# Kernel optimization log

Hardware: AMD Instinct MI355X
Metric: run time of the kernel (lower is better)

The kernel has to match this reference:

```python
import jax, jax.numpy as jnp
import numpy as np

N, D_IN, D_H, D_OUT = 65536, 256, 256, 128
E, TOP_K = 16, 2


def setup_inputs() -> dict:
    key = jax.random.key(0)
    ks = jax.random.split(key, 16)
    s = 0.05
    inp = {
        'x': jax.random.normal(ks[0], (N, D_IN), jnp.float32),
        'W0': jax.random.normal(ks[1], (D_IN, D_H), jnp.float32) * s,
        'b0': jnp.zeros((D_H,), jnp.float32),
        'Wg1': jax.random.normal(ks[2], (D_H, E), jnp.float32) * s,
        'bg1': jnp.zeros((E,), jnp.float32),
        'We1': jax.random.normal(ks[3], (E, D_H, D_H), jnp.float32) * s,
        'be1': jnp.zeros((E, D_H), jnp.float32),
        'Wg2': jax.random.normal(ks[4], (D_H, E), jnp.float32) * s,
        'bg2': jnp.zeros((E,), jnp.float32),
        'We2': jax.random.normal(ks[5], (E, D_H, D_H), jnp.float32) * s,
        'be2': jnp.zeros((E, D_H), jnp.float32),
        'Wf': jax.random.normal(ks[6], (D_H, D_OUT), jnp.float32) * s,
        'bf': jnp.zeros((D_OUT,), jnp.float32),
    }
    return inp


def _moe_layer(h, Wg, bg, We, be):
    # naive gate: logits over experts, top-k, renormalized softmax of top-k vals
    logits = h @ Wg + bg                      # [N, E]
    gate_full = jax.nn.softmax(logits, axis=-1)  # returned 'gate' for std stat
    vals, idx = jax.lax.top_k(logits, TOP_K)  # [N, k]
    scores = jax.nn.softmax(vals, axis=-1)    # [N, k]
    # scatter top-k scores into dense combine weights [N, E]
    cw = (jax.nn.one_hot(idx, E, dtype=h.dtype) * scores[..., None]).sum(axis=1)
    # grouped GEMM expressed as masked per-expert GEMMs (E is small, fixed)
    y = jnp.zeros((h.shape[0], We.shape[-1]), h.dtype)
    for e in range(E):
        y = y + cw[:, e:e + 1] * (h @ We[e] + be[e])
    # torch.std defaults to unbiased (ddof=1)
    gate_std_mean = jnp.std(gate_full, axis=1, ddof=1).mean()
    return y, gate_std_mean


def reference(x, W0, b0, Wg1, bg1, We1, be1, Wg2, bg2, We2, be2, Wf, bf):
    h = jax.nn.relu(x @ W0 + b0)
    h, g1 = _moe_layer(h, Wg1, bg1, We1, be1)
    h = jax.nn.relu(h)
    h, g2 = _moe_layer(h, Wg2, bg2, We2, be2)
    h = jax.nn.relu(h)
    out = h @ Wf + bf
    gate_std_means_mean = (g1 + g2) * 0.5
    return out, gate_std_means_mean
```

## Files before the change

kernel.cpp:

```cpp
#include <hip/hip_runtime.h>
#include <math.h>

#define NT 65536
#define DH 256
#define DO 128
#define NE 16
#define MAXCH 528
#define CPX 66

struct RInfo { int e1, e2; float s1, s2; };

typedef __attribute__((ext_vector_type(8))) short bh8;
typedef __attribute__((ext_vector_type(4))) float fx4;

static __device__ __forceinline__ short f2bf(float f) {
    union { float f; unsigned u; } v; v.f = f;
    return (short)((v.u + 0x7FFFu + ((v.u >> 16) & 1u)) >> 16);
}

template<bool RELU>
__global__ __launch_bounds__(256)
void gemm_dense(const float* __restrict__ A, const float* __restrict__ B,
                const float* __restrict__ bias, float* __restrict__ C,
                int ncols)
{
    __shared__ float As[128][36];
    __shared__ float Bs[32][132];
    const int tid = threadIdx.x;
    const int tx = tid & 15, ty = tid >> 4;
    const int rowBase = blockIdx.x * 128;
    const int colBase = blockIdx.y * 128;

    float acc[8][8];
#pragma unroll
    for (int i = 0; i < 8; ++i)
#pragma unroll
        for (int j = 0; j < 8; ++j) acc[i][j] = 0.f;

    for (int kt = 0; kt < DH; kt += 32) {
        {
            const int r = tid >> 3, k4 = (tid & 7) << 2;
#pragma unroll
            for (int it = 0; it < 4; ++it) {
                const float4 v = *reinterpret_cast<const float4*>(
                    &A[(size_t)(rowBase + r + 32 * it) * DH + kt + k4]);
                *reinterpret_cast<float4*>(&As[r + 32 * it][k4]) = v;
            }
        }
        {
            const int kr = tid >> 5, c4 = (tid & 31) << 2;
#pragma unroll
            for (int it = 0; it < 4; ++it) {
                const float4 v = *reinterpret_cast<const float4*>(
                    &B[(size_t)(kt + kr + 8 * it) * ncols + colBase + c4]);
                *reinterpret_cast<float4*>(&Bs[kr + 8 * it][c4]) = v;
            }
        }
        __syncthreads();
#pragma unroll
        for (int k4 = 0; k4 < 32; k4 += 4) {
            alignas(16) float ar[8][4];
#pragma unroll
            for (int i = 0; i < 8; ++i)
                *reinterpret_cast<float4*>(ar[i]) =
                    *reinterpret_cast<const float4*>(&As[ty * 8 + i][k4]);
#pragma unroll
            for (int kk = 0; kk < 4; ++kk) {
                alignas(16) float br[8];
                *reinterpret_cast<float4*>(&br[0]) =
                    *reinterpret_cast<const float4*>(&Bs[k4 + kk][tx * 8]);
                *reinterpret_cast<float4*>(&br[4]) =
                    *reinterpret_cast<const float4*>(&Bs[k4 + kk][tx * 8 + 4]);
#pragma unroll
                for (int i = 0; i < 8; ++i) {
                    const float a = ar[i][kk];
#pragma unroll
                    for (int j = 0; j < 8; ++j)
                        acc[i][j] = fmaf(a, br[j], acc[i][j]);
                }
            }
        }
        __syncthreads();
    }
    alignas(16) float bb[8];
#pragma unroll
    for (int j = 0; j < 8; ++j) bb[j] = bias[colBase + tx * 8 + j];
#pragma unroll
    for (int i = 0; i < 8; ++i) {
        const size_t row = rowBase + ty * 8 + i;
        alignas(16) float o[8];
#pragma unroll
        for (int j = 0; j < 8; ++j) {
            float v = acc[i][j] + bb[j];
            if (RELU) v = fmaxf(v, 0.f);
            o[j] = v;
        }
        float* p = &C[row * (size_t)ncols + colBase + tx * 8];
        *reinterpret_cast<float4*>(p)     = *reinterpret_cast<float4*>(&o[0]);
        *reinterpret_cast<float4*>(p + 4) = *reinterpret_cast<float4*>(&o[4]);
    }
}

__global__ __launch_bounds__(256)
void gate_kernel(const float* __restrict__ H, const float* __restrict__ Wg,
                 const float* __restrict__ bg, RInfo* __restrict__ info,
                 float* gsum, int* __restrict__ bc0, int* __restrict__ bc1)
{
    __shared__ float wgsT[16][260];
    __shared__ float hs[16][260];
    __shared__ float lg[16][17];
    __shared__ float sbg[16];
    __shared__ float sds[16];
    __shared__ int hh0[NE], hh1[NE];
    const int tid = threadIdx.x;
    const int rowBase = blockIdx.x * 16;

#pragma unroll
    for (int it = 0; it < 4; ++it) {
        const int flat = (tid + 256 * it) * 4;
        const int k = flat >> 4, e4 = flat & 15;
        const float4 v = *reinterpret_cast<const float4*>(&Wg[flat]);
        wgsT[e4 + 0][k] = v.x;
        wgsT[e4 + 1][k] = v.y;
        wgsT[e4 + 2][k] = v.z;
        wgsT[e4 + 3][k] = v.w;
    }
    if (tid < 16) { sbg[tid] = bg[tid]; hh0[tid] = 0; hh1[tid] = 0; }
#pragma unroll
    for (int it = 0; it < 4; ++it) {
        const int flat = (tid + 256 * it) * 4;
        const int r = flat >> 8, k = flat & 255;
        *reinterpret_cast<float4*>(&hs[r][k]) =
            *reinterpret_cast<const float4*>(&H[(size_t)(rowBase + r) * DH + k]);
    }
    __syncthreads();
    {
        const int r = tid >> 4, e = tid & 15;
        float acc = 0.f;
#pragma unroll 8
        for (int k = 0; k < 256; k += 4) {
            const float4 hv = *reinterpret_cast<const float4*>(&hs[r][k]);
            const float4 wv = *reinterpret_cast<const float4*>(&wgsT[e][k]);
            acc = fmaf(hv.x, wv.x, acc);
            acc = fmaf(hv.y, wv.y, acc);
            acc = fmaf(hv.z, wv.z, acc);
            acc = fmaf(hv.w, wv.w, acc);
        }
        lg[r][e] = acc + sbg[e];
    }
    __syncthreads();
    if (tid < 16) {
        const int row = rowBase + tid;
        float l[16];
#pragma unroll
        for (int i = 0; i < 16; ++i) l[i] = lg[tid][i];
        int i1 = 0; float v1 = l[0];
#pragma unroll
        for (int i = 1; i < 16; ++i) if (l[i] > v1) { v1 = l[i]; i1 = i; }
        int i2 = -1; float v2 = -INFINITY;
#pragma unroll
        for (int i = 0; i < 16; ++i) if (i != i1 && l[i] > v2) { v2 = l[i]; i2 = i; }
        const float t = expf(v2 - v1);
        const float s1 = 1.f / (1.f + t);
        const float s2 = t / (1.f + t);
        float p[16]; float S = 0.f;
#pragma unroll
        for (int i = 0; i < 16; ++i) { p[i] = expf(l[i] - v1); S += p[i]; }
        const float inv = 1.f / S;
        float sq = 0.f;
#pragma unroll
        for (int i = 0; i < 16; ++i) { const float q = p[i] * inv; sq = fmaf(q, q, sq); }
        const float var = (sq - 1.0f / 16.0f) * (1.0f / 15.0f);
        const float sd = sqrtf(fmaxf(var, 0.f));

        RInfo ri; ri.e1 = i1; ri.e2 = i2; ri.s1 = s1; ri.s2 = s2;
        info[row] = ri;
        sds[tid] = sd;
        atomicAdd(&hh0[i1], 1);
        atomicAdd(&hh1[i2], 1);
    }
    __syncthreads();
    if (tid == 0) {
        float s = 0.f;
#pragma unroll
        for (int i = 0; i < 16; ++i) s += sds[i];
        atomicAdd(gsum, s);
    }
    if (tid < 16) {
        const int b = blockIdx.x >> 4;
        if (hh0[tid]) atomicAdd(&bc0[tid * 256 + b], hh0[tid]);
        if (hh1[tid]) atomicAdd(&bc1[tid * 256 + b], hh1[tid]);
    }
}

__global__ void zero_meta(int* bc0, int* bc1, float* gsum)
{
    const int idx = blockIdx.x * 256 + threadIdx.x;
    bc0[idx] = 0; bc1[idx] = 0;
    if (idx < 2) gsum[idx] = 0.f;
}

__global__ void scan2_kernel(int* __restrict__ bc0, int* __restrict__ bc1,
                             int* cnt0, int* cnt1, int* off0, int* off1,
                             int* __restrict__ bo0, int* __restrict__ bo1)
{
    __shared__ int tot0[NE], tot1[NE], base0[NE], base1[NE];
    const int t = threadIdx.x;
    if (t < NE) {
        int s = 0;
        for (int b = 0; b < 256; ++b) s += bc0[t * 256 + b];
        tot0[t] = s; cnt0[t] = s;
    } else if (t < 2 * NE) {
        const int e = t - NE;
        int s = 0;
        for (int b = 0; b < 256; ++b) s += bc1[e * 256 + b];
        tot1[e] = s; cnt1[e] = s;
    }
    __syncthreads();
    if (t == 0) { int a = 0; for (int e = 0; e < NE; ++e) { base0[e] = a; off0[e] = a; a += tot0[e]; } }
    if (t == 1) { int a = 0; for (int e = 0; e < NE; ++e) { base1[e] = a; off1[e] = a; a += tot1[e]; } }
    __syncthreads();
    if (t < NE) {
        int run = base0[t];
        for (int b = 0; b < 256; ++b) { bo0[t * 256 + b] = run; run += bc0[t * 256 + b]; }
    } else if (t < 2 * NE) {
        const int e = t - NE;
        int run = base1[e];
        for (int b = 0; b < 256; ++b) { bo1[e * 256 + b] = run; run += bc1[e * 256 + b]; }
    }
    __syncthreads();
    for (int i = t; i < NE * 256; i += 64) { bc0[i] = 0; bc1[i] = 0; }
}

__global__ __launch_bounds__(256)
void scatter2_kernel(const RInfo* __restrict__ info, const int* __restrict__ bo0,
                     const int* __restrict__ bo1, int* __restrict__ l0,
                     int* __restrict__ l1)
{
    __shared__ int h0[NE], h1[NE];
    const int tid = threadIdx.x, b = blockIdx.x;
    if (tid < NE) { h0[tid] = 0; h1[tid] = 0; }
    __syncthreads();
    const int r = b * 256 + tid;
    const RInfo ri = info[r];
    const int p0 = atomicAdd(&h0[ri.e1], 1);
    const int p1 = atomicAdd(&h1[ri.e2], 1);
    l0[bo0[ri.e1 * 256 + b] + p0] = r;
    l1[bo1[ri.e2 * 256 + b] + p1] = r;
}

template<int SLOT>
__global__ __launch_bounds__(256)
void gemm_expert(const float* __restrict__ Hin, const float* __restrict__ We,
                 const float* __restrict__ be, const RInfo* __restrict__ info,
                 const int* __restrict__ list, const int* __restrict__ cnts,
                 const int* __restrict__ offs, float* __restrict__ P,
                 short* __restrict__ Ybf)
{
    __shared__ float As[128][36];
    __shared__ float Bs[32][132];
    __shared__ int   rs[128];
    __shared__ float ss[128];

    int c = (blockIdx.x & 7) * CPX + (blockIdx.x >> 3);
    int e;
    int cnt = 0;
    for (e = 0; e < NE; ++e) {
        cnt = cnts[e];
        const int nch = (cnt + 127) >> 7;
        if (c < nch) break;
        c -= nch;
    }
    if (e >= NE) return;
    const int m = min(128, cnt - c * 128);
    const int base = offs[e] + c * 128;
    const int tid = threadIdx.x;
    const int tx = tid & 15, ty = tid >> 4;
    const int colBase = blockIdx.y * 128;

    if (tid < 128) {
        const int g = list[base + min(tid, m - 1)];
        rs[tid] = g;
        const RInfo ri = info[g];
        ss[tid] = (SLOT == 0) ? ri.s1 : ri.s2;
    }
    __syncthreads();

    const float* B = We + (size_t)e * DH * DH;

    float acc[8][8];
#pragma unroll
    for (int i = 0; i < 8; ++i)
#pragma unroll
        for (int j = 0; j < 8; ++j) acc[i][j] = 0.f;

    for (int kt = 0; kt < DH; kt += 32) {
        {
            const int r = tid >> 3, k4 = (tid & 7) << 2;
#pragma unroll
            for (int it = 0; it < 4; ++it) {
                const int g = rs[r + 32 * it];
                const float4 v = *reinterpret_cast<const float4*>(
                    &Hin[(size_t)g * DH + kt + k4]);
                *reinterpret_cast<float4*>(&As[r + 32 * it][k4]) = v;
            }
        }
        {
            const int kr = tid >> 5, c4 = (tid & 31) << 2;
#pragma unroll
            for (int it = 0; it < 4; ++it) {
                const float4 v = *reinterpret_cast<const float4*>(
                    &B[(size_t)(kt + kr + 8 * it) * DH + colBase + c4]);
                *reinterpret_cast<float4*>(&Bs[kr + 8 * it][c4]) = v;
            }
        }
        __syncthreads();
#pragma unroll
        for (int k4 = 0; k4 < 32; k4 += 4) {
            alignas(16) float ar[8][4];
#pragma unroll
            for (int i = 0; i < 8; ++i)
                *reinterpret_cast<float4*>(ar[i]) =
                    *reinterpret_cast<const float4*>(&As[ty * 8 + i][k4]);
#pragma unroll
            for (int kk = 0; kk < 4; ++kk) {
                alignas(16) float br[8];
                *reinterpret_cast<float4*>(&br[0]) =
                    *reinterpret_cast<const float4*>(&Bs[k4 + kk][tx * 8]);
                *reinterpret_cast<float4*>(&br[4]) =
                    *reinterpret_cast<const float4*>(&Bs[k4 + kk][tx * 8 + 4]);
#pragma unroll
                for (int i = 0; i < 8; ++i) {
                    const float a = ar[i][kk];
#pragma unroll
                    for (int j = 0; j < 8; ++j)
                        acc[i][j] = fmaf(a, br[j], acc[i][j]);
                }
            }
        }
        __syncthreads();
    }

    alignas(16) float bb[8];
#pragma unroll
    for (int j = 0; j < 8; ++j) bb[j] = be[(size_t)e * DH + colBase + tx * 8 + j];
#pragma unroll
    for (int i = 0; i < 8; ++i) {
        const int rl = ty * 8 + i;
        if (rl < m) {
            const int g = rs[rl];
            const float s = ss[rl];
            alignas(16) float o[8];
#pragma unroll
            for (int j = 0; j < 8; ++j) o[j] = s * (acc[i][j] + bb[j]);
            float* pp = &P[(size_t)g * DH + colBase + tx * 8];
            if (SLOT == 0) {
                *reinterpret_cast<float4*>(pp)     = *reinterpret_cast<float4*>(&o[0]);
                *reinterpret_cast<float4*>(pp + 4) = *reinterpret_cast<float4*>(&o[4]);
            } else {
                const float4 p0 = *reinterpret_cast<const float4*>(pp);
                const float4 p1 = *reinterpret_cast<const float4*>(pp + 4);
                alignas(16) float h[8];
                h[0] = fmaxf(o[0] + p0.x, 0.f); h[1] = fmaxf(o[1] + p0.y, 0.f);
                h[2] = fmaxf(o[2] + p0.z, 0.f); h[3] = fmaxf(o[3] + p0.w, 0.f);
                h[4] = fmaxf(o[4] + p1.x, 0.f); h[5] = fmaxf(o[5] + p1.y, 0.f);
                h[6] = fmaxf(o[6] + p1.z, 0.f); h[7] = fmaxf(o[7] + p1.w, 0.f);
                *reinterpret_cast<float4*>(pp)     = *reinterpret_cast<float4*>(&h[0]);
                *reinterpret_cast<float4*>(pp + 4) = *reinterpret_cast<float4*>(&h[4]);
                if (Ybf) {
                    bh8 yb;
#pragma unroll
                    for (int j = 0; j < 8; ++j) yb[j] = f2bf(h[j]);
                    *reinterpret_cast<bh8*>(&Ybf[(size_t)g * DH + colBase + tx * 8]) = yb;
                }
            }
        }
    }
}

__global__ __launch_bounds__(256)
void transp_bf16(const float* __restrict__ W, short* __restrict__ WT,
                 int K, int N)
{
    __shared__ float t[32][33];
    const int k0 = blockIdx.x * 32, n0 = blockIdx.y * 32;
    const size_t off = (size_t)blockIdx.z * K * N;
    const int c = threadIdx.x & 31, r8 = threadIdx.x >> 5;
#pragma unroll
    for (int it = 0; it < 4; ++it) {
        const int r = r8 + it * 8;
        t[r][c] = W[off + (size_t)(k0 + r) * N + n0 + c];
    }
    __syncthreads();
#pragma unroll
    for (int it = 0; it < 4; ++it) {
        const int r = r8 + it * 8;
        WT[off + (size_t)(n0 + r) * K + k0 + c] = f2bf(t[c][r]);
    }
}

template<int SLOT, int BFA>
__global__ __launch_bounds__(256)
void gemm_expert_bf16(const float* __restrict__ Yf, const short* __restrict__ Abf,
                      const short* __restrict__ WeT,
                      const float* __restrict__ be, const RInfo* __restrict__ info,
                      const int* __restrict__ list, const int* __restrict__ cnts,
                      const int* __restrict__ offs, float* __restrict__ P,
                      short* __restrict__ Hbf)
{
    __shared__ bh8 As8[512];
    __shared__ bh8 Bs8[512];
    __shared__ int   rs[128];
    __shared__ float ss[128];

    int c = (blockIdx.x & 7) * CPX + (blockIdx.x >> 3);
    int e;
    int cnt = 0;
    for (e = 0; e < NE; ++e) {
        cnt = cnts[e];
        const int nch = (cnt + 127) >> 7;
        if (c < nch) break;
        c -= nch;
    }
    if (e >= NE) return;
    const int m = min(128, cnt - c * 128);
    const int base = offs[e] + c * 128;
    const int tid = threadIdx.x;

    if (tid < 128) {
        const int g = list[base + min(tid, m - 1)];
        rs[tid] = g;
        const RInfo ri = info[g];
        ss[tid] = (SLOT == 0) ? ri.s1 : ri.s2;
    }
    __syncthreads();

    const int colBase = blockIdx.y * 128;
    const int lane = tid & 63, wave = tid >> 6;
    const int wr = wave >> 1, wc = wave & 1;
    const short* Bw = WeT + (size_t)e * DH * DH;

    fx4 acc[4][4];
    const fx4 z = {0.f, 0.f, 0.f, 0.f};
#pragma unroll
    for (int i = 0; i < 4; ++i)
#pragma unroll
        for (int j = 0; j < 4; ++j) acc[i][j] = z;

    const int d0 = tid, d1 = tid + 256;
    const int ar0 = d0 >> 2, ak0 = d0 & 3;
    const int ar1 = d1 >> 2, ak1 = d1 & 3;
    const int g0 = ar0 * 4 + (ak0 ^ ((ar0 >> 1) & 3));
    const int g1 = ar1 * 4 + (ak1 ^ ((ar1 >> 1) & 3));
    const size_t arow0 = (size_t)rs[ar0] * DH, arow1 = (size_t)rs[ar1] * DH;
    const size_t brow0 = (size_t)(colBase + ar0) * DH, brow1 = (size_t)(colBase + ar1) * DH;

    for (int kt = 0; kt < DH; kt += 32) {
        if (BFA) {
            As8[g0] = *reinterpret_cast<const bh8*>(&Abf[arow0 + kt + ak0 * 8]);
            As8[g1] = *reinterpret_cast<const bh8*>(&Abf[arow1 + kt + ak1 * 8]);
        } else {
            const float* s0 = &Yf[arow0 + kt + ak0 * 8];
            const float4 f0 = *reinterpret_cast<const float4*>(s0);
            const float4 f1 = *reinterpret_cast<const float4*>(s0 + 4);
            bh8 v;
            v[0]=f2bf(f0.x); v[1]=f2bf(f0.y); v[2]=f2bf(f0.z); v[3]=f2bf(f0.w);
            v[4]=f2bf(f1.x); v[5]=f2bf(f1.y); v[6]=f2bf(f1.z); v[7]=f2bf(f1.w);
            As8[g0] = v;
            const float* s1 = &Yf[arow1 + kt + ak1 * 8];
            const float4 f2 = *reinterpret_cast<const float4*>(s1);
            const float4 f3 = *reinterpret_cast<const float4*>(s1 + 4);
            bh8 w;
            w[0]=f2bf(f2.x); w[1]=f2bf(f2.y); w[2]=f2bf(f2.z); w[3]=f2bf(f2.w);
            w[4]=f2bf(f3.x); w[5]=f2bf(f3.y); w[6]=f2bf(f3.z); w[7]=f2bf(f3.w);
            As8[g1] = w;
        }
        {
            Bs8[g0] = *reinterpret_cast<const bh8*>(&Bw[brow0 + kt + ak0 * 8]);
            Bs8[g1] = *reinterpret_cast<const bh8*>(&Bw[brow1 + kt + ak1 * 8]);
        }
        __syncthreads();
        const int kq = lane >> 4, lm = lane & 15;
        bh8 af[4], bfr[4];
#pragma unroll
        for (int i = 0; i < 4; ++i) {
            const int rl = wr * 64 + i * 16 + lm;
            af[i] = As8[rl * 4 + (kq ^ ((rl >> 1) & 3))];
            const int cl = wc * 64 + i * 16 + lm;
            bfr[i] = Bs8[cl * 4 + (kq ^ ((cl >> 1) & 3))];
        }
#pragma unroll
        for (int i = 0; i < 4; ++i)
#pragma unroll
            for (int j = 0; j < 4; ++j)
                acc[i][j] = __builtin_amdgcn_mfma_f32_16x16x32_bf16(
                    af[i], bfr[j], acc[i][j], 0, 0, 0);
        __syncthreads();
    }

    const int rq = lane >> 4, lm = lane & 15;
#pragma unroll
    for (int i = 0; i < 4; ++i) {
#pragma unroll
        for (int j = 0; j < 4; ++j) {
            const int rl = wr * 64 + i * 16 + rq * 4 + j;
            if (rl < m) {
                const int g = rs[rl];
                const float s = ss[rl];
#pragma unroll
                for (int nf = 0; nf < 4; ++nf) {
                    const int cl = colBase + wc * 64 + nf * 16 + lm;
                    float* pp = &P[(size_t)g * DH + cl];
                    const float o = s * (acc[i][nf][j] + be[(size_t)e * DH + cl]);
                    if (SLOT == 0) {
                        *pp = o;
                    } else {
                        const float v = fmaxf(*pp + o, 0.f);
                        if (BFA) Hbf[(size_t)g * DH + cl] = f2bf(v);
                        else     *pp = v;
                    }
                }
            }
        }
    }
}

template<int BFA>
__global__ __launch_bounds__(256)
void gemm_final_bf16(const float* __restrict__ Hf, const short* __restrict__ Habf,
                     const short* __restrict__ WT,
                     const float* __restrict__ bias, float* __restrict__ C,
                     const float* gsum, float* scalar_out)
{
    __shared__ bh8 As8[512];
    __shared__ bh8 Bs8[512];
    const int tid = threadIdx.x;
    const int rowBase = blockIdx.x * 128;

    if (blockIdx.x == 0 && tid == 0)
        *scalar_out = (gsum[0] + gsum[1]) * (0.5f / (float)NT);

    const int lane = tid & 63, wave = tid >> 6;
    const int wr = wave >> 1, wc = wave & 1;

    fx4 acc[4][4];
    const fx4 z = {0.f, 0.f, 0.f, 0.f};
#pragma unroll
    for (int i = 0; i < 4; ++i)
#pragma unroll
        for (int j = 0; j < 4; ++j) acc[i][j] = z;

    const int d0 = tid, d1 = tid + 256;
    const int ar0 = d0 >> 2, ak0 = d0 & 3;
    const int ar1 = d1 >> 2, ak1 = d1 & 3;
    const int g0 = ar0 * 4 + (ak0 ^ ((ar0 >> 1) & 3));
    const int g1 = ar1 * 4 + (ak1 ^ ((ar1 >> 1) & 3));
    const size_t arow0 = (size_t)(rowBase + ar0) * DH, arow1 = (size_t)(rowBase + ar1) * DH;
    const size_t brow0 = (size_t)ar0 * DH, brow1 = (size_t)ar1 * DH;

    for (int kt = 0; kt < DH; kt += 32) {
        if (BFA) {
            As8[g0] = *reinterpret_cast<const bh8*>(&Habf[arow0 + kt + ak0 * 8]);
            As8[g1] = *reinterpret_cast<const bh8*>(&Habf[arow1 + kt + ak1 * 8]);
        } else {
            const float* s0 = &Hf[arow0 + kt + ak0 * 8];
            const float4 f0 = *reinterpret_cast<const float4*>(s0);
            const float4 f1 = *reinterpret_cast<const float4*>(s0 + 4);
            bh8 v;
            v[0]=f2bf(f0.x); v[1]=f2bf(f0.y); v[2]=f2bf(f0.z); v[3]=f2bf(f0.w);
            v[4]=f2bf(f1.x); v[5]=f2bf(f1.y); v[6]=f2bf(f1.z); v[7]=f2bf(f1.w);
            As8[g0] = v;
            const float* s1 = &Hf[arow1 + kt + ak1 * 8];
            const float4 f2 = *reinterpret_cast<const float4*>(s1);
            const float4 f3 = *reinterpret_cast<const float4*>(s1 + 4);
            bh8 w;
            w[0]=f2bf(f2.x); w[1]=f2bf(f2.y); w[2]=f2bf(f2.z); w[3]=f2bf(f2.w);
            w[4]=f2bf(f3.x); w[5]=f2bf(f3.y); w[6]=f2bf(f3.z); w[7]=f2bf(f3.w);
            As8[g1] = w;
        }
        {
            Bs8[g0] = *reinterpret_cast<const bh8*>(&WT[brow0 + kt + ak0 * 8]);
            Bs8[g1] = *reinterpret_cast<const bh8*>(&WT[brow1 + kt + ak1 * 8]);
        }
        __syncthreads();
        const int kq = lane >> 4, lm = lane & 15;
        bh8 af[4], bfr[4];
#pragma unroll
        for (int i = 0; i < 4; ++i) {
            const int rl = wr * 64 + i * 16 + lm;
            af[i] = As8[rl * 4 + (kq ^ ((rl >> 1) & 3))];
            const int cl = wc * 64 + i * 16 + lm;
            bfr[i] = Bs8[cl * 4 + (kq ^ ((cl >> 1) & 3))];
        }
#pragma unroll
        for (int i = 0; i < 4; ++i)
#pragma unroll
            for (int j = 0; j < 4; ++j)
                acc[i][j] = __builtin_amdgcn_mfma_f32_16x16x32_bf16(
                    af[i], bfr[j], acc[i][j], 0, 0, 0);
        __syncthreads();
    }

    const int rq = lane >> 4, lm = lane & 15;
#pragma unroll
    for (int i = 0; i < 4; ++i) {
#pragma unroll
        for (int j = 0; j < 4; ++j) {
            const int rl = rowBase + wr * 64 + i * 16 + rq * 4 + j;
#pragma unroll
            for (int nf = 0; nf < 4; ++nf) {
                const int cl = wc * 64 + nf * 16 + lm;
                C[(size_t)rl * DO + cl] = acc[i][nf][j] + bias[cl];
            }
        }
    }
}

extern "C" void kernel_launch(void* const* d_in, const int* in_sizes, int n_in,
                              void* d_out, int out_size, void* d_ws, size_t ws_size,
                              hipStream_t stream)
{
    const float* x   = (const float*)d_in[0];
    const float* W0  = (const float*)d_in[1];
    const float* b0  = (const float*)d_in[2];
    const float* Wg1 = (const float*)d_in[3];
    const float* bg1 = (const float*)d_in[4];
    const float* We1 = (const float*)d_in[5];
    const float* be1 = (const float*)d_in[6];
    const float* Wg2 = (const float*)d_in[7];
    const float* bg2 = (const float*)d_in[8];
    const float* We2 = (const float*)d_in[9];
    const float* be2 = (const float*)d_in[10];
    const float* Wf  = (const float*)d_in[11];
    const float* bf  = (const float*)d_in[12];
    float* out = (float*)d_out;

    char* w = (char*)d_ws;
    float* H    = (float*)w; w += (size_t)NT * DH * 4;
    float* Y    = (float*)w; w += (size_t)NT * DH * 4;
    RInfo* info = (RInfo*)w; w += (size_t)NT * sizeof(RInfo);
    int* l0   = (int*)w; w += (size_t)NT * 4;
    int* l1   = (int*)w; w += (size_t)NT * 4;
    int* bc0  = (int*)w; w += NE * 256 * 4;
    int* bc1  = (int*)w; w += NE * 256 * 4;
    int* bo0  = (int*)w; w += NE * 256 * 4;
    int* bo1  = (int*)w; w += NE * 256 * 4;
    int* cnt0 = (int*)w; w += 64;
    int* cnt1 = (int*)w; w += 64;
    int* off0 = (int*)w; w += 64;
    int* off1 = (int*)w; w += 64;
    float* gsum = (float*)w; w += 64;
    short* WeT = (short*)w; w += (size_t)NE * DH * DH * 2;
    short* WfT = (short*)w; w += (size_t)DH * DO * 2;
    short* Ybf = (short*)w; w += (size_t)NT * DH * 2;
    const bool roomy = (size_t)(w - (char*)d_ws) <= ws_size;
    short* Hbf = (short*)Y;

    zero_meta<<<dim3(16), dim3(256), 0, stream>>>(bc0, bc1, gsum);
    transp_bf16<<<dim3(8, 8, 16), dim3(256), 0, stream>>>(We2, WeT, DH, DH);
    transp_bf16<<<dim3(8, 4, 1),  dim3(256), 0, stream>>>(Wf,  WfT, DH, DO);

    gemm_dense<true><<<dim3(NT / 128, 2), dim3(256), 0, stream>>>(x, W0, b0, H, DH);

    gate_kernel<<<dim3(NT / 16), dim3(256), 0, stream>>>(H, Wg1, bg1, info, &gsum[0], bc0, bc1);
    scan2_kernel<<<dim3(1), dim3(64), 0, stream>>>(bc0, bc1, cnt0, cnt1, off0, off1, bo0, bo1);
    scatter2_kernel<<<dim3(NT / 256), dim3(256), 0, stream>>>(info, bo0, bo1, l0, l1);
    gemm_expert<0><<<dim3(MAXCH, 2), dim3(256), 0, stream>>>(H, We1, be1, info, l0, cnt0, off0, Y, nullptr);
    gemm_expert<1><<<dim3(MAXCH, 2), dim3(256), 0, stream>>>(H, We1, be1, info, l1, cnt1, off1, Y,
                                                             roomy ? Ybf : nullptr);

    gate_kernel<<<dim3(NT / 16), dim3(256), 0, stream>>>(Y, Wg2, bg2, info, &gsum[1], bc0, bc1);
    scan2_kernel<<<dim3(1), dim3(64), 0, stream>>>(bc0, bc1, cnt0, cnt1, off0, off1, bo0, bo1);
    scatter2_kernel<<<dim3(NT / 256), dim3(256), 0, stream>>>(info, bo0, bo1, l0, l1);
    if (roomy) {
        gemm_expert_bf16<0,1><<<dim3(MAXCH, 2), dim3(256), 0, stream>>>(Y, Ybf, WeT, be2, info, l0, cnt0, off0, H, nullptr);
        gemm_expert_bf16<1,1><<<dim3(MAXCH, 2), dim3(256), 0, stream>>>(Y, Ybf, WeT, be2, info, l1, cnt1, off1, H, Hbf);
        gemm_final_bf16<1><<<dim3(NT / 128), dim3(256), 0, stream>>>(H, Hbf, WfT, bf, out, gsum, out + (size_t)NT * DO);
    } else {
        gemm_expert_bf16<0,0><<<dim3(MAXCH, 2), dim3(256), 0, stream>>>(Y, nullptr, WeT, be2, info, l0, cnt0, off0, H, nullptr);
        gemm_expert_bf16<1,0><<<dim3(MAXCH, 2), dim3(256), 0, stream>>>(Y, nullptr, WeT, be2, info, l1, cnt1, off1, H, nullptr);
        gemm_final_bf16<0><<<dim3(NT / 128), dim3(256), 0, stream>>>(H, nullptr, WfT, bf, out, gsum, out + (size_t)NT * DO);
    }
}
```

Before: 603.5 us.

## Double-buffer LDS tiles in bf16 GEMMs and process 32 rows per gate block

The bf16 expert GEMM and the final GEMM now keep two LDS buffers. Global loads for the next K tile are issued into registers before the MFMAs on the current tile and stored to the other buffer afterwards, which hides global-load latency and removes one barrier per iteration. The gate kernel now handles 32 rows per block instead of 16, which halves the block count and the per-block Wg transpose loads. Block-to-bucket indexing is adjusted to match. The cost is higher LDS and register use, which may lower occupancy.

```diff
diff --git a/kernel.cpp b/kernel.cpp
--- a/kernel.cpp
+++ b/kernel.cpp
@@ -107,13 +107,13 @@
                  float* gsum, int* __restrict__ bc0, int* __restrict__ bc1)
 {
     __shared__ float wgsT[16][260];
-    __shared__ float hs[16][260];
-    __shared__ float lg[16][17];
+    __shared__ float hs[32][260];
+    __shared__ float lg[32][17];
     __shared__ float sbg[16];
-    __shared__ float sds[16];
+    __shared__ float sds[32];
     __shared__ int hh0[NE], hh1[NE];
     const int tid = threadIdx.x;
-    const int rowBase = blockIdx.x * 16;
+    const int rowBase = blockIdx.x * 32;
 
 #pragma unroll
     for (int it = 0; it < 4; ++it) {
@@ -127,15 +127,16 @@
     }
     if (tid < 16) { sbg[tid] = bg[tid]; hh0[tid] = 0; hh1[tid] = 0; }
 #pragma unroll
-    for (int it = 0; it < 4; ++it) {
+    for (int it = 0; it < 8; ++it) {
         const int flat = (tid + 256 * it) * 4;
         const int r = flat >> 8, k = flat & 255;
         *reinterpret_cast<float4*>(&hs[r][k]) =
             *reinterpret_cast<const float4*>(&H[(size_t)(rowBase + r) * DH + k]);
     }
     __syncthreads();
-    {
-        const int r = tid >> 4, e = tid & 15;
+#pragma unroll
+    for (int rr = 0; rr < 2; ++rr) {
+        const int r = (tid >> 4) + 16 * rr, e = tid & 15;
         float acc = 0.f;
 #pragma unroll 8
         for (int k = 0; k < 256; k += 4) {
@@ -149,7 +150,7 @@
         lg[r][e] = acc + sbg[e];
     }
     __syncthreads();
-    if (tid < 16) {
+    if (tid < 32) {
         const int row = rowBase + tid;
         float l[16];
 #pragma unroll
@@ -183,11 +184,11 @@
     if (tid == 0) {
         float s = 0.f;
 #pragma unroll
-        for (int i = 0; i < 16; ++i) s += sds[i];
+        for (int i = 0; i < 32; ++i) s += sds[i];
         atomicAdd(gsum, s);
     }
     if (tid < 16) {
-        const int b = blockIdx.x >> 4;
+        const int b = blockIdx.x >> 3;
         if (hh0[tid]) atomicAdd(&bc0[tid * 256 + b], hh0[tid]);
         if (hh1[tid]) atomicAdd(&bc1[tid * 256 + b], hh1[tid]);
     }
@@ -408,8 +409,8 @@
                       const int* __restrict__ offs, float* __restrict__ P,
                       short* __restrict__ Hbf)
 {
-    __shared__ bh8 As8[512];
-    __shared__ bh8 Bs8[512];
+    __shared__ bh8 As8[2][512];
+    __shared__ bh8 Bs8[2][512];
     __shared__ int   rs[128];
     __shared__ float ss[128];
 
@@ -455,39 +456,56 @@
     const size_t arow0 = (size_t)rs[ar0] * DH, arow1 = (size_t)rs[ar1] * DH;
     const size_t brow0 = (size_t)(colBase + ar0) * DH, brow1 = (size_t)(colBase + ar1) * DH;
 
-    for (int kt = 0; kt < DH; kt += 32) {
-        if (BFA) {
-            As8[g0] = *reinterpret_cast<const bh8*>(&Abf[arow0 + kt + ak0 * 8]);
-            As8[g1] = *reinterpret_cast<const bh8*>(&Abf[arow1 + kt + ak1 * 8]);
-        } else {
-            const float* s0 = &Yf[arow0 + kt + ak0 * 8];
-            const float4 f0 = *reinterpret_cast<const float4*>(s0);
-            const float4 f1 = *reinterpret_cast<const float4*>(s0 + 4);
-            bh8 v;
-            v[0]=f2bf(f0.x); v[1]=f2bf(f0.y); v[2]=f2bf(f0.z); v[3]=f2bf(f0.w);
-            v[4]=f2bf(f1.x); v[5]=f2bf(f1.y); v[6]=f2bf(f1.z); v[7]=f2bf(f1.w);
-            As8[g0] = v;
-            const float* s1 = &Yf[arow1 + kt + ak1 * 8];
-            const float4 f2 = *reinterpret_cast<const float4*>(s1);
-            const float4 f3 = *reinterpret_cast<const float4*>(s1 + 4);
-            bh8 w;
-            w[0]=f2bf(f2.x); w[1]=f2bf(f2.y); w[2]=f2bf(f2.z); w[3]=f2bf(f2.w);
-            w[4]=f2bf(f3.x); w[5]=f2bf(f3.y); w[6]=f2bf(f3.z); w[7]=f2bf(f3.w);
-            As8[g1] = w;
-        }
-        {
-            Bs8[g0] = *reinterpret_cast<const bh8*>(&Bw[brow0 + kt + ak0 * 8]);
-            Bs8[g1] = *reinterpret_cast<const bh8*>(&Bw[brow1 + kt + ak1 * 8]);
-        }
-        __syncthreads();
+    if (BFA) {
+        As8[0][g0] = *reinterpret_cast<const bh8*>(&Abf[arow0 + ak0 * 8]);
+        As8[0][g1] = *reinterpret_cast<const bh8*>(&Abf[arow1 + ak1 * 8]);
+    } else {
+        const float4 f0 = *reinterpret_cast<const float4*>(&Yf[arow0 + ak0 * 8]);
+        const float4 f1 = *reinterpret_cast<const float4*>(&Yf[arow0 + ak0 * 8 + 4]);
+        bh8 v;
+        v[0]=f2bf(f0.x); v[1]=f2bf(f0.y); v[2]=f2bf(f0.z); v[3]=f2bf(f0.w);
+        v[4]=f2bf(f1.x); v[5]=f2bf(f1.y); v[6]=f2bf(f1.z); v[7]=f2bf(f1.w);
+        As8[0][g0] = v;
+        const float4 f2 = *reinterpret_cast<const float4*>(&Yf[arow1 + ak1 * 8]);
+        const float4 f3 = *reinterpret_cast<const float4*>(&Yf[arow1 + ak1 * 8 + 4]);
+        bh8 w;
+        w[0]=f2bf(f2.x); w[1]=f2bf(f2.y); w[2]=f2bf(f2.z); w[3]=f2bf(f2.w);
+        w[4]=f2bf(f3.x); w[5]=f2bf(f3.y); w[6]=f2bf(f3.z); w[7]=f2bf(f3.w);
+        As8[0][g1] = w;
+    }
+    Bs8[0][g0] = *reinterpret_cast<const bh8*>(&Bw[brow0 + ak0 * 8]);
+    Bs8[0][g1] = *reinterpret_cast<const bh8*>(&Bw[brow1 + ak1 * 8]);
+    __syncthreads();
+
+    for (int kti = 0; kti < 8; ++kti) {
+        const int cur = kti & 1;
+        const int ktn = (kti + 1) * 32;
+        const bool more = (kti < 7);
+
+        bh8 pA0, pA1, pb0, pb1;
+        float4 fa0, fa1, fa2, fa3;
+        if (more) {
+            if (BFA) {
+                pA0 = *reinterpret_cast<const bh8*>(&Abf[arow0 + ktn + ak0 * 8]);
+                pA1 = *reinterpret_cast<const bh8*>(&Abf[arow1 + ktn + ak1 * 8]);
+            } else {
+                fa0 = *reinterpret_cast<const float4*>(&Yf[arow0 + ktn + ak0 * 8]);
+                fa1 = *reinterpret_cast<const float4*>(&Yf[arow0 + ktn + ak0 * 8 + 4]);
+                fa2 = *reinterpret_cast<const float4*>(&Yf[arow1 + ktn + ak1 * 8]);
+                fa3 = *reinterpret_cast<const float4*>(&Yf[arow1 + ktn + ak1 * 8 + 4]);
+            }
+            pb0 = *reinterpret_cast<const bh8*>(&Bw[brow0 + ktn + ak0 * 8]);
+            pb1 = *reinterpret_cast<const bh8*>(&Bw[brow1 + ktn + ak1 * 8]);
+        }
+
         const int kq = lane >> 4, lm = lane & 15;
         bh8 af[4], bfr[4];
 #pragma unroll
         for (int i = 0; i < 4; ++i) {
             const int rl = wr * 64 + i * 16 + lm;
-            af[i] = As8[rl * 4 + (kq ^ ((rl >> 1) & 3))];
+            af[i] = As8[cur][rl * 4 + (kq ^ ((rl >> 1) & 3))];
             const int cl = wc * 64 + i * 16 + lm;
-            bfr[i] = Bs8[cl * 4 + (kq ^ ((cl >> 1) & 3))];
+            bfr[i] = Bs8[cur][cl * 4 + (kq ^ ((cl >> 1) & 3))];
         }
 #pragma unroll
         for (int i = 0; i < 4; ++i)
@@ -495,6 +513,24 @@
             for (int j = 0; j < 4; ++j)
                 acc[i][j] = __builtin_amdgcn_mfma_f32_16x16x32_bf16(
                     af[i], bfr[j], acc[i][j], 0, 0, 0);
+
+        if (more) {
+            if (BFA) {
+                As8[cur ^ 1][g0] = pA0;
+                As8[cur ^ 1][g1] = pA1;
+            } else {
+                bh8 v;
+                v[0]=f2bf(fa0.x); v[1]=f2bf(fa0.y); v[2]=f2bf(fa0.z); v[3]=f2bf(fa0.w);
+                v[4]=f2bf(fa1.x); v[5]=f2bf(fa1.y); v[6]=f2bf(fa1.z); v[7]=f2bf(fa1.w);
+                As8[cur ^ 1][g0] = v;
+                bh8 w;
+                w[0]=f2bf(fa2.x); w[1]=f2bf(fa2.y); w[2]=f2bf(fa2.z); w[3]=f2bf(fa2.w);
+                w[4]=f2bf(fa3.x); w[5]=f2bf(fa3.y); w[6]=f2bf(fa3.z); w[7]=f2bf(fa3.w);
+                As8[cur ^ 1][g1] = w;
+            }
+            Bs8[cur ^ 1][g0] = pb0;
+            Bs8[cur ^ 1][g1] = pb1;
+        }
         __syncthreads();
     }
 
@@ -532,8 +568,8 @@
                      const float* __restrict__ bias, float* __restrict__ C,
                      const float* gsum, float* scalar_out)
 {
-    __shared__ bh8 As8[512];
-    __shared__ bh8 Bs8[512];
+    __shared__ bh8 As8[2][512];
+    __shared__ bh8 Bs8[2][512];
     const int tid = threadIdx.x;
     const int rowBase = blockIdx.x * 128;
 
@@ -558,39 +594,56 @@
     const size_t arow0 = (size_t)(rowBase + ar0) * DH, arow1 = (size_t)(rowBase + ar1) * DH;
     const size_t brow0 = (size_t)ar0 * DH, brow1 = (size_t)ar1 * DH;
 
-    for (int kt = 0; kt < DH; kt += 32) {
-        if (BFA) {
-            As8[g0] = *reinterpret_cast<const bh8*>(&Habf[arow0 + kt + ak0 * 8]);
-            As8[g1] = *reinterpret_cast<const bh8*>(&Habf[arow1 + kt + ak1 * 8]);
-        } else {
-            const float* s0 = &Hf[arow0 + kt + ak0 * 8];
-            const float4 f0 = *reinterpret_cast<const float4*>(s0);
-            const float4 f1 = *reinterpret_cast<const float4*>(s0 + 4);
-            bh8 v;
-            v[0]=f2bf(f0.x); v[1]=f2bf(f0.y); v[2]=f2bf(f0.z); v[3]=f2bf(f0.w);
-            v[4]=f2bf(f1.x); v[5]=f2bf(f1.y); v[6]=f2bf(f1.z); v[7]=f2bf(f1.w);
-            As8[g0] = v;
-            const float* s1 = &Hf[arow1 + kt + ak1 * 8];
-            const float4 f2 = *reinterpret_cast<const float4*>(s1);
-            const float4 f3 = *reinterpret_cast<const float4*>(s1 + 4);
-            bh8 w;
-            w[0]=f2bf(f2.x); w[1]=f2bf(f2.y); w[2]=f2bf(f2.z); w[3]=f2bf(f2.w);
-            w[4]=f2bf(f3.x); w[5]=f2bf(f3.y); w[6]=f2bf(f3.z); w[7]=f2bf(f3.w);
-            As8[g1] = w;
-        }
-        {
-            Bs8[g0] = *reinterpret_cast<const bh8*>(&WT[brow0 + kt + ak0 * 8]);
-            Bs8[g1] = *reinterpret_cast<const bh8*>(&WT[brow1 + kt + ak1 * 8]);
-        }
-        __syncthreads();
+    if (BFA) {
+        As8[0][g0] = *reinterpret_cast<const bh8*>(&Habf[arow0 + ak0 * 8]);
+        As8[0][g1] = *reinterpret_cast<const bh8*>(&Habf[arow1 + ak1 * 8]);
+    } else {
+        const float4 f0 = *reinterpret_cast<const float4*>(&Hf[arow0 + ak0 * 8]);
+        const float4 f1 = *reinterpret_cast<const float4*>(&Hf[arow0 + ak0 * 8 + 4]);
+        bh8 v;
+        v[0]=f2bf(f0.x); v[1]=f2bf(f0.y); v[2]=f2bf(f0.z); v[3]=f2bf(f0.w);
+        v[4]=f2bf(f1.x); v[5]=f2bf(f1.y); v[6]=f2bf(f1.z); v[7]=f2bf(f1.w);
+        As8[0][g0] = v;
+        const float4 f2 = *reinterpret_cast<const float4*>(&Hf[arow1 + ak1 * 8]);
+        const float4 f3 = *reinterpret_cast<const float4*>(&Hf[arow1 + ak1 * 8 + 4]);
+        bh8 w;
+        w[0]=f2bf(f2.x); w[1]=f2bf(f2.y); w[2]=f2bf(f2.z); w[3]=f2bf(f2.w);
+        w[4]=f2bf(f3.x); w[5]=f2bf(f3.y); w[6]=f2bf(f3.z); w[7]=f2bf(f3.w);
+        As8[0][g1] = w;
+    }
+    Bs8[0][g0] = *reinterpret_cast<const bh8*>(&WT[brow0 + ak0 * 8]);
+    Bs8[0][g1] = *reinterpret_cast<const bh8*>(&WT[brow1 + ak1 * 8]);
+    __syncthreads();
+
+    for (int kti = 0; kti < 8; ++kti) {
+        const int cur = kti & 1;
+        const int ktn = (kti + 1) * 32;
+        const bool more = (kti < 7);
+
+        bh8 pA0, pA1, pb0, pb1;
+        float4 fa0, fa1, fa2, fa3;
+        if (more) {
+            if (BFA) {
+                pA0 = *reinterpret_cast<const bh8*>(&Habf[arow0 + ktn + ak0 * 8]);
+                pA1 = *reinterpret_cast<const bh8*>(&Habf[arow1 + ktn + ak1 * 8]);
+            } else {
+                fa0 = *reinterpret_cast<const float4*>(&Hf[arow0 + ktn + ak0 * 8]);
+                fa1 = *reinterpret_cast<const float4*>(&Hf[arow0 + ktn + ak0 * 8 + 4]);
+                fa2 = *reinterpret_cast<const float4*>(&Hf[arow1 + ktn + ak1 * 8]);
+                fa3 = *reinterpret_cast<const float4*>(&Hf[arow1 + ktn + ak1 * 8 + 4]);
+            }
+            pb0 = *reinterpret_cast<const bh8*>(&WT[brow0 + ktn + ak0 * 8]);
+            pb1 = *reinterpret_cast<const bh8*>(&WT[brow1 + ktn + ak1 * 8]);
+        }
+
         const int kq = lane >> 4, lm = lane & 15;
         bh8 af[4], bfr[4];
 #pragma unroll
         for (int i = 0; i < 4; ++i) {
             const int rl = wr * 64 + i * 16 + lm;
-            af[i] = As8[rl * 4 + (kq ^ ((rl >> 1) & 3))];
+            af[i] = As8[cur][rl * 4 + (kq ^ ((rl >> 1) & 3))];
             const int cl = wc * 64 + i * 16 + lm;
-            bfr[i] = Bs8[cl * 4 + (kq ^ ((cl >> 1) & 3))];
+            bfr[i] = Bs8[cur][cl * 4 + (kq ^ ((cl >> 1) & 3))];
         }
 #pragma unroll
         for (int i = 0; i < 4; ++i)
@@ -598,6 +651,24 @@
             for (int j = 0; j < 4; ++j)
                 acc[i][j] = __builtin_amdgcn_mfma_f32_16x16x32_bf16(
                     af[i], bfr[j], acc[i][j], 0, 0, 0);
+
+        if (more) {
+            if (BFA) {
+                As8[cur ^ 1][g0] = pA0;
+                As8[cur ^ 1][g1] = pA1;
+            } else {
+                bh8 v;
+                v[0]=f2bf(fa0.x); v[1]=f2bf(fa0.y); v[2]=f2bf(fa0.z); v[3]=f2bf(fa0.w);
+                v[4]=f2bf(fa1.x); v[5]=f2bf(fa1.y); v[6]=f2bf(fa1.z); v[7]=f2bf(fa1.w);
+                As8[cur ^ 1][g0] = v;
+                bh8 w;
+                w[0]=f2bf(fa2.x); w[1]=f2bf(fa2.y); w[2]=f2bf(fa2.z); w[3]=f2bf(fa2.w);
+                w[4]=f2bf(fa3.x); w[5]=f2bf(fa3.y); w[6]=f2bf(fa3.z); w[7]=f2bf(fa3.w);
+                As8[cur ^ 1][g1] = w;
+            }
+            Bs8[cur ^ 1][g0] = pb0;
+            Bs8[cur ^ 1][g1] = pb1;
+        }
         __syncthreads();
     }
 
@@ -662,14 +733,14 @@
 
     gemm_dense<true><<<dim3(NT / 128, 2), dim3(256), 0, stream>>>(x, W0, b0, H, DH);
 
-    gate_kernel<<<dim3(NT / 16), dim3(256), 0, stream>>>(H, Wg1, bg1, info, &gsum[0], bc0, bc1);
+    gate_kernel<<<dim3(NT / 32), dim3(256), 0, stream>>>(H, Wg1, bg1, info, &gsum[0], bc0, bc1);
     scan2_kernel<<<dim3(1), dim3(64), 0, stream>>>(bc0, bc1, cnt0, cnt1, off0, off1, bo0, bo1);
     scatter2_kernel<<<dim3(NT / 256), dim3(256), 0, stream>>>(info, bo0, bo1, l0, l1);
     gemm_expert<0><<<dim3(MAXCH, 2), dim3(256), 0, stream>>>(H, We1, be1, info, l0, cnt0, off0, Y, nullptr);
     gemm_expert<1><<<dim3(MAXCH, 2), dim3(256), 0, stream>>>(H, We1, be1, info, l1, cnt1, off1, Y,
                                                              roomy ? Ybf : nullptr);
 
-    gate_kernel<<<dim3(NT / 16), dim3(256), 0, stream>>>(Y, Wg2, bg2, info, &gsum[1], bc0, bc1);
+    gate_kernel<<<dim3(NT / 32), dim3(256), 0, stream>>>(Y, Wg2, bg2, info, &gsum[1], bc0, bc1);
     scan2_kernel<<<dim3(1), dim3(64), 0, stream>>>(bc0, bc1, cnt0, cnt1, off0, off1, bo0, bo1);
     scatter2_kernel<<<dim3(NT / 256), dim3(256), 0, stream>>>(info, bo0, bo1, l0, l1);
     if (roomy) {
```

Measured after the change: 557.4 us (median of 2 runs). -7.6%, faster.
